# Kernel optimization log

Measured on AMD Instinct MI355X. Metric: run time of the kernel, lower is better.

## Reference

```python
import jax, jax.numpy as jnp
import numpy as np

N_NODES = 50000
N_EDGES = 800000
IN_FEATS = 512
NUM_HEADS = 4
OUT_FEATS = 64
NEG_SLOPE = 0.2


def setup_inputs() -> dict:
    key = jax.random.key(0)
    k1, k2, k3, k4, k5, k6 = jax.random.split(key, 6)
    feat = jax.random.normal(k1, (N_NODES, IN_FEATS), dtype=jnp.float32)
    W = jax.random.normal(k2, (IN_FEATS, NUM_HEADS * OUT_FEATS), dtype=jnp.float32) * (1.0 / np.sqrt(IN_FEATS))
    attn_l = jax.random.normal(k3, (NUM_HEADS, OUT_FEATS), dtype=jnp.float32) * (1.0 / np.sqrt(OUT_FEATS))
    attn_r = jax.random.normal(k4, (NUM_HEADS, OUT_FEATS), dtype=jnp.float32) * (1.0 / np.sqrt(OUT_FEATS))
    src = jax.random.randint(k5, (N_EDGES,), 0, N_NODES, dtype=jnp.int32)
    dst = jax.random.randint(k6, (N_EDGES,), 0, N_NODES, dtype=jnp.int32)
    return {"feat": feat, "W": W, "attn_l": attn_l, "attn_r": attn_r, "src": src, "dst": dst}


def reference(feat, W, attn_l, attn_r, src, dst):
    N = feat.shape[0]
    H, D = attn_l.shape
    # node-wise projection: fc(feat).view(N, H, D)
    ft = (feat @ W).reshape(N, H, D)
    # per-node attention logits
    el = jnp.einsum('nhd,hd->nh', ft, attn_l)  # [N, H]
    er = jnp.einsum('nhd,hd->nh', ft, attn_r)  # [N, H]
    # edge-wise score: leaky_relu(el[u] + er[v])
    e = jax.nn.leaky_relu(el[src] + er[dst], negative_slope=NEG_SLOPE)  # [E, H]
    # segment softmax over incoming edges of each destination node
    e_max = jax.ops.segment_max(e, dst, num_segments=N)  # [N, H]
    e_max = jnp.where(jnp.isfinite(e_max), e_max, 0.0)
    exp_e = jnp.exp(e - e_max[dst])  # [E, H]
    denom = jax.ops.segment_sum(exp_e, dst, num_segments=N)  # [N, H]
    a = exp_e / denom[dst]  # [E, H]
    # weighted message aggregation: sum_u a(u,v) * ft[u]
    msg = ft[src] * a[:, :, None]  # [E, H, D]
    out = jax.ops.segment_sum(msg, dst, num_segments=N)  # [N, H, D]
    return out.reshape(N, H * D)
```

## Files before the change

### kernel.cpp

```cpp
#include <hip/hip_runtime.h>

#define N_NODES 50000
#define N_EDGES 800000
#define IN_F    512
#define NH      4
#define DH      64
#define HD      256
#define NEG     0.2f
#define NB      ((N_NODES + 255) / 256)

typedef __attribute__((ext_vector_type(8))) short bf16x8;
typedef __attribute__((ext_vector_type(4))) float f32x4;

__device__ __forceinline__ unsigned short f2bf(float x) {
    unsigned u = __float_as_uint(x);
    unsigned r = (u + 0x7FFFu + ((u >> 16) & 1u)) >> 16;
    return (unsigned short)r;
}
__device__ __forceinline__ float bf2f(unsigned short b) {
    return __uint_as_float((unsigned)b << 16);
}

__global__ __launch_bounds__(256) void setup_kernel(const float* __restrict__ W,
                                                    unsigned short* __restrict__ WtbT,
                                                    int* __restrict__ counts) {
    int b = blockIdx.x;
    if (b < NB) {
        int i = b * 256 + threadIdx.x;
        if (i < N_NODES) counts[i] = 0;
    } else {
        int i = (b - NB) * 256 + threadIdx.x;
        if (i < IN_F * HD) {
            int k = i >> 8;
            int n = i & 255;
            int t  = k >> 6;
            int kk = k & 63;
            int g  = kk >> 3;
            int w8 = kk & 7;
            int p  = n * 8 + (g ^ (n & 7));
            WtbT[(size_t)t * 16384 + p * 8 + w8] = f2bf(W[i]);
        }
    }
}

__global__ __launch_bounds__(256) void count_kernel(const int* __restrict__ dst,
                                                    int* __restrict__ counts) {
    int e = blockIdx.x * blockDim.x + threadIdx.x;
    if (e < N_EDGES) atomicAdd(&counts[dst[e]], 1);
}

#define LDPA 72
__global__ __launch_bounds__(256) void gemm_kernel(const float* __restrict__ A,
                                                   const unsigned short* __restrict__ WtbT,
                                                   const float* __restrict__ attn_l,
                                                   const float* __restrict__ attn_r,
                                                   unsigned short* __restrict__ Cb,
                                                   float* __restrict__ el,
                                                   float* __restrict__ er) {
    __shared__ short A_s[64][LDPA];
    __shared__ short B_s[2][256 * 64];

    const int tid  = threadIdx.x;
    const int lane = tid & 63;
    const int w    = tid >> 6;
    const int lm   = lane & 15;
    const int quad = lane >> 4;
    const int row0 = blockIdx.x * 64;

    const int srow = tid >> 3;
    const int sc8  = (tid & 7) * 8;

    f32x4 acc[4][4] = {};
    float4 pa[4];

#define STAGE_B(BUF, T)                                                         \
    {                                                                           \
        const char* gsrc = (const char*)WtbT + (size_t)(T) * 32768 + tid * 16;  \
        char* ldst = (char*)&B_s[BUF][0] + tid * 16;                            \
        _Pragma("unroll")                                                       \
        for (int r = 0; r < 8; r++)                                             \
            __builtin_amdgcn_global_load_lds(                                   \
                (const __attribute__((address_space(1))) unsigned int*)(gsrc + r * 4096), \
                (__attribute__((address_space(3))) unsigned int*)(ldst + r * 4096),       \
                16, 0, 0);                                                      \
    }

#define LOAD_A(KT)                                                             \
    {                                                                          \
        int g0 = row0 + srow;                                                  \
        if (g0 < N_NODES) {                                                    \
            const float* ap = A + (size_t)g0 * IN_F + (KT) + sc8;              \
            pa[0] = *(const float4*)ap; pa[1] = *(const float4*)(ap + 4);      \
        } else { pa[0] = pa[1] = make_float4(0.f, 0.f, 0.f, 0.f); }            \
        int g1 = row0 + 32 + srow;                                             \
        if (g1 < N_NODES) {                                                    \
            const float* ap = A + (size_t)g1 * IN_F + (KT) + sc8;              \
            pa[2] = *(const float4*)ap; pa[3] = *(const float4*)(ap + 4);      \
        } else { pa[2] = pa[3] = make_float4(0.f, 0.f, 0.f, 0.f); }            \
    }

    STAGE_B(0, 0);
    LOAD_A(0);

    int buf = 0;
    for (int t = 0; t < 8; t++) {
        {
            bf16x8 s;
            s[0] = (short)f2bf(pa[0].x); s[1] = (short)f2bf(pa[0].y);
            s[2] = (short)f2bf(pa[0].z); s[3] = (short)f2bf(pa[0].w);
            s[4] = (short)f2bf(pa[1].x); s[5] = (short)f2bf(pa[1].y);
            s[6] = (short)f2bf(pa[1].z); s[7] = (short)f2bf(pa[1].w);
            *(bf16x8*)(&A_s[srow][sc8]) = s;
            s[0] = (short)f2bf(pa[2].x); s[1] = (short)f2bf(pa[2].y);
            s[2] = (short)f2bf(pa[2].z); s[3] = (short)f2bf(pa[2].w);
            s[4] = (short)f2bf(pa[3].x); s[5] = (short)f2bf(pa[3].y);
            s[6] = (short)f2bf(pa[3].z); s[7] = (short)f2bf(pa[3].w);
            *(bf16x8*)(&A_s[32 + srow][sc8]) = s;
        }
        __syncthreads();

        if (t + 1 < 8) { STAGE_B(buf ^ 1, t + 1); LOAD_A((t + 1) * 64); }

#pragma unroll
        for (int kk = 0; kk < 64; kk += 32) {
            bf16x8 af[4], bfr[4];
#pragma unroll
            for (int i = 0; i < 4; i++)
                af[i] = *(const bf16x8*)(&A_s[i * 16 + lm][kk + quad * 8]);
#pragma unroll
            for (int j = 0; j < 4; j++) {
                int n  = w * 64 + j * 16 + lm;
                int g  = (kk >> 3) + quad;
                int gs = g ^ (lm & 7);
                bfr[j] = *(const bf16x8*)(&B_s[buf][(n * 8 + gs) * 8]);
            }
#pragma unroll
            for (int i = 0; i < 4; i++)
#pragma unroll
                for (int j = 0; j < 4; j++)
                    acc[i][j] = __builtin_amdgcn_mfma_f32_16x16x32_bf16(
                        af[i], bfr[j], acc[i][j], 0, 0, 0);
        }
        if (t < 7) __syncthreads();
        buf ^= 1;
    }
#undef LOAD_A
#undef STAGE_B

#pragma unroll
    for (int i = 0; i < 4; i++) {
#pragma unroll
        for (int j = 0; j < 4; j++) {
            int gcol = w * 64 + j * 16 + lm;
#pragma unroll
            for (int r = 0; r < 4; r++) {
                int grow = row0 + i * 16 + quad * 4 + r;
                if (grow < N_NODES)
                    Cb[(size_t)grow * HD + gcol] = f2bf(acc[i][j][r]);
            }
        }
    }

    {
        float al[4], ar[4];
#pragma unroll
        for (int j = 0; j < 4; j++) {
            al[j] = attn_l[w * DH + j * 16 + lm];
            ar[j] = attn_r[w * DH + j * 16 + lm];
        }
#pragma unroll
        for (int i = 0; i < 4; i++) {
#pragma unroll
            for (int r = 0; r < 4; r++) {
                float sl = 0.f, sr = 0.f;
#pragma unroll
                for (int j = 0; j < 4; j++) {
                    sl += acc[i][j][r] * al[j];
                    sr += acc[i][j][r] * ar[j];
                }
#pragma unroll
                for (int off = 8; off > 0; off >>= 1) {
                    sl += __shfl_xor(sl, off);
                    sr += __shfl_xor(sr, off);
                }
                if (lm == 0) {
                    int grow = row0 + i * 16 + quad * 4 + r;
                    if (grow < N_NODES) {
                        el[(size_t)grow * NH + w] = sl;
                        er[(size_t)grow * NH + w] = sr;
                    }
                }
            }
        }
    }
}

__global__ __launch_bounds__(256) void partial_kernel(const int* __restrict__ counts,
                                                      int* __restrict__ bsums) {
    __shared__ int red[4];
    int i = blockIdx.x * 256 + threadIdx.x;
    int c = (i < N_NODES) ? counts[i] : 0;
#pragma unroll
    for (int off = 32; off > 0; off >>= 1) c += __shfl_down(c, off);
    if ((threadIdx.x & 63) == 0) red[threadIdx.x >> 6] = c;
    __syncthreads();
    if (threadIdx.x == 0) bsums[blockIdx.x] = red[0] + red[1] + red[2] + red[3];
}

__global__ __launch_bounds__(256) void bscan_kernel(const int* __restrict__ bsums,
                                                    int* __restrict__ boffs) {
    __shared__ int s[256];
    int tid = threadIdx.x;
    s[tid] = (tid < NB) ? bsums[tid] : 0;
    __syncthreads();
    for (int off = 1; off < 256; off <<= 1) {
        int x = s[tid];
        int a = (tid >= off) ? s[tid - off] : 0;
        __syncthreads();
        s[tid] = x + a;
        __syncthreads();
    }
    if (tid < NB) boffs[tid] = (tid > 0) ? s[tid - 1] : 0;
}

__global__ __launch_bounds__(256) void scatter_scan_kernel(const int* __restrict__ counts,
                                                           const int* __restrict__ boffs,
                                                           int* __restrict__ offsets,
                                                           int* __restrict__ cursor) {
    __shared__ int s[256];
    int tid = threadIdx.x;
    int i = blockIdx.x * 256 + tid;
    s[tid] = (i < N_NODES) ? counts[i] : 0;
    __syncthreads();
    for (int off = 1; off < 256; off <<= 1) {
        int x = s[tid];
        int a = (tid >= off) ? s[tid - off] : 0;
        __syncthreads();
        s[tid] = x + a;
        __syncthreads();
    }
    int excl = (tid > 0) ? s[tid - 1] : 0;
    int o = boffs[blockIdx.x] + excl;
    if (i < N_NODES) { offsets[i] = o; cursor[i] = o; }
    if (i == 0) offsets[N_NODES] = N_EDGES;
}

__global__ __launch_bounds__(256) void edge_place_kernel(const int* __restrict__ src,
                                                         const int* __restrict__ dst,
                                                         int* __restrict__ cursor,
                                                         int* __restrict__ srcs) {
    int e = blockIdx.x * blockDim.x + threadIdx.x;
    if (e >= N_EDGES) return;
    int u = src[e], v = dst[e];
    int pos = atomicAdd(&cursor[v], 1);
    srcs[pos] = u;
}

__device__ __forceinline__ float lrelu_exp(float x) {
    float y = fmaxf(x, NEG * x);
    return __expf(y);
}

__global__ __launch_bounds__(256) void agg_kernel(const unsigned short* __restrict__ ftb,
                                                  const float* __restrict__ el,
                                                  const float* __restrict__ er,
                                                  const int* __restrict__ srcs,
                                                  const int* __restrict__ offsets,
                                                  float* __restrict__ out) {
    int wv   = (blockIdx.x * blockDim.x + threadIdx.x) >> 6;
    int lane = threadIdx.x & 63;
    if (wv >= N_NODES) return;

    const int beg = offsets[wv];
    const int end = offsets[wv + 1];
    const int h   = lane >> 4;
    const size_t foff = (size_t)lane * 4;
    const float erv = er[(size_t)wv * NH + h];

    float4 acc = make_float4(0.f, 0.f, 0.f, 0.f);
    float dsum = 0.f;

    const int n8 = (end - beg) >> 3;
    int u0, u1, u2, u3, u4, u5, u6, u7;
    if (n8 > 0) {
        const int* sp = srcs + beg;
        u0 = sp[0]; u1 = sp[1]; u2 = sp[2]; u3 = sp[3];
        u4 = sp[4]; u5 = sp[5]; u6 = sp[6]; u7 = sp[7];
        for (int b = 0; b < n8; b++) {
            const int base = beg + b * 8;
            int v0 = 0, v1 = 0, v2 = 0, v3 = 0, v4 = 0, v5 = 0, v6 = 0, v7 = 0;
            if (b + 1 < n8) {
                const int* np = srcs + base + 8;
                v0 = np[0]; v1 = np[1]; v2 = np[2]; v3 = np[3];
                v4 = np[4]; v5 = np[5]; v6 = np[6]; v7 = np[7];
            }
            ushort4 f0 = *(const ushort4*)(ftb + (size_t)u0 * HD + foff);
            ushort4 f1 = *(const ushort4*)(ftb + (size_t)u1 * HD + foff);
            ushort4 f2 = *(const ushort4*)(ftb + (size_t)u2 * HD + foff);
            ushort4 f3 = *(const ushort4*)(ftb + (size_t)u3 * HD + foff);
            ushort4 f4 = *(const ushort4*)(ftb + (size_t)u4 * HD + foff);
            ushort4 f5 = *(const ushort4*)(ftb + (size_t)u5 * HD + foff);
            ushort4 f6 = *(const ushort4*)(ftb + (size_t)u6 * HD + foff);
            ushort4 f7 = *(const ushort4*)(ftb + (size_t)u7 * HD + foff);
            float e0 = el[(size_t)u0 * NH + h];
            float e1 = el[(size_t)u1 * NH + h];
            float e2 = el[(size_t)u2 * NH + h];
            float e3 = el[(size_t)u3 * NH + h];
            float e4 = el[(size_t)u4 * NH + h];
            float e5 = el[(size_t)u5 * NH + h];
            float e6 = el[(size_t)u6 * NH + h];
            float e7 = el[(size_t)u7 * NH + h];
            float w0 = lrelu_exp(e0 + erv), w1 = lrelu_exp(e1 + erv);
            float w2 = lrelu_exp(e2 + erv), w3 = lrelu_exp(e3 + erv);
            float w4 = lrelu_exp(e4 + erv), w5 = lrelu_exp(e5 + erv);
            float w6 = lrelu_exp(e6 + erv), w7 = lrelu_exp(e7 + erv);
            acc.x += w0 * bf2f(f0.x) + w1 * bf2f(f1.x) + w2 * bf2f(f2.x) + w3 * bf2f(f3.x)
                   + w4 * bf2f(f4.x) + w5 * bf2f(f5.x) + w6 * bf2f(f6.x) + w7 * bf2f(f7.x);
            acc.y += w0 * bf2f(f0.y) + w1 * bf2f(f1.y) + w2 * bf2f(f2.y) + w3 * bf2f(f3.y)
                   + w4 * bf2f(f4.y) + w5 * bf2f(f5.y) + w6 * bf2f(f6.y) + w7 * bf2f(f7.y);
            acc.z += w0 * bf2f(f0.z) + w1 * bf2f(f1.z) + w2 * bf2f(f2.z) + w3 * bf2f(f3.z)
                   + w4 * bf2f(f4.z) + w5 * bf2f(f5.z) + w6 * bf2f(f6.z) + w7 * bf2f(f7.z);
            acc.w += w0 * bf2f(f0.w) + w1 * bf2f(f1.w) + w2 * bf2f(f2.w) + w3 * bf2f(f3.w)
                   + w4 * bf2f(f4.w) + w5 * bf2f(f5.w) + w6 * bf2f(f6.w) + w7 * bf2f(f7.w);
            dsum += ((w0 + w1) + (w2 + w3)) + ((w4 + w5) + (w6 + w7));
            u0 = v0; u1 = v1; u2 = v2; u3 = v3;
            u4 = v4; u5 = v5; u6 = v6; u7 = v7;
        }
    }
    {
        const int p0  = beg + n8 * 8;
        const int rem = end - p0;
        if (rem > 0) {
            const int* sp = srcs + p0;
            int x0 = sp[0];
            int x1 = (1 < rem) ? sp[1] : x0;
            int x2 = (2 < rem) ? sp[2] : x0;
            int x3 = (3 < rem) ? sp[3] : x0;
            int x4 = (4 < rem) ? sp[4] : x0;
            int x5 = (5 < rem) ? sp[5] : x0;
            int x6 = (6 < rem) ? sp[6] : x0;
            ushort4 f0 = *(const ushort4*)(ftb + (size_t)x0 * HD + foff);
            ushort4 f1 = *(const ushort4*)(ftb + (size_t)x1 * HD + foff);
            ushort4 f2 = *(const ushort4*)(ftb + (size_t)x2 * HD + foff);
            ushort4 f3 = *(const ushort4*)(ftb + (size_t)x3 * HD + foff);
            ushort4 f4 = *(const ushort4*)(ftb + (size_t)x4 * HD + foff);
            ushort4 f5 = *(const ushort4*)(ftb + (size_t)x5 * HD + foff);
            ushort4 f6 = *(const ushort4*)(ftb + (size_t)x6 * HD + foff);
            float e0 = el[(size_t)x0 * NH + h];
            float e1 = el[(size_t)x1 * NH + h];
            float e2 = el[(size_t)x2 * NH + h];
            float e3 = el[(size_t)x3 * NH + h];
            float e4 = el[(size_t)x4 * NH + h];
            float e5 = el[(size_t)x5 * NH + h];
            float e6 = el[(size_t)x6 * NH + h];
            float w0 = lrelu_exp(e0 + erv);
            float w1 = (1 < rem) ? lrelu_exp(e1 + erv) : 0.f;
            float w2 = (2 < rem) ? lrelu_exp(e2 + erv) : 0.f;
            float w3 = (3 < rem) ? lrelu_exp(e3 + erv) : 0.f;
            float w4 = (4 < rem) ? lrelu_exp(e4 + erv) : 0.f;
            float w5 = (5 < rem) ? lrelu_exp(e5 + erv) : 0.f;
            float w6 = (6 < rem) ? lrelu_exp(e6 + erv) : 0.f;
            acc.x += w0 * bf2f(f0.x) + w1 * bf2f(f1.x) + w2 * bf2f(f2.x) + w3 * bf2f(f3.x)
                   + w4 * bf2f(f4.x) + w5 * bf2f(f5.x) + w6 * bf2f(f6.x);
            acc.y += w0 * bf2f(f0.y) + w1 * bf2f(f1.y) + w2 * bf2f(f2.y) + w3 * bf2f(f3.y)
                   + w4 * bf2f(f4.y) + w5 * bf2f(f5.y) + w6 * bf2f(f6.y);
            acc.z += w0 * bf2f(f0.z) + w1 * bf2f(f1.z) + w2 * bf2f(f2.z) + w3 * bf2f(f3.z)
                   + w4 * bf2f(f4.z) + w5 * bf2f(f5.z) + w6 * bf2f(f6.z);
            acc.w += w0 * bf2f(f0.w) + w1 * bf2f(f1.w) + w2 * bf2f(f2.w) + w3 * bf2f(f3.w)
                   + w4 * bf2f(f4.w) + w5 * bf2f(f5.w) + w6 * bf2f(f6.w);
            dsum += ((w0 + w1) + (w2 + w3)) + ((w4 + w5) + w6);
        }
    }

    float inv = (dsum > 0.f) ? (1.f / dsum) : 0.f;
    acc.x *= inv; acc.y *= inv; acc.z *= inv; acc.w *= inv;
    *(float4*)(out + (size_t)wv * HD + foff) = acc;
}

extern "C" void kernel_launch(void* const* d_in, const int* in_sizes, int n_in,
                              void* d_out, int out_size, void* d_ws, size_t ws_size,
                              hipStream_t stream) {
    const float* feat   = (const float*)d_in[0];
    const float* W      = (const float*)d_in[1];
    const float* attn_l = (const float*)d_in[2];
    const float* attn_r = (const float*)d_in[3];
    const int*   src    = (const int*)d_in[4];
    const int*   dst    = (const int*)d_in[5];
    float* out = (float*)d_out;

    char* p = (char*)d_ws;
    auto alloc = [&](size_t bytes) -> char* {
        char* r = p;
        p += (bytes + 255) & ~(size_t)255;
        return r;
    };
    unsigned short* ftb     = (unsigned short*)alloc((size_t)N_NODES * HD * 2);
    unsigned short* WtbT    = (unsigned short*)alloc((size_t)IN_F * HD * 2);
    float*          el      = (float*)alloc((size_t)N_NODES * NH * 4);
    float*          er      = (float*)alloc((size_t)N_NODES * NH * 4);
    int*            srcs    = (int*)alloc((size_t)N_EDGES * 4);
    int*            counts  = (int*)alloc((size_t)N_NODES * 4);
    int*            offsets = (int*)alloc((size_t)(N_NODES + 1) * 4);
    int*            cursor  = (int*)alloc((size_t)N_NODES * 4);
    int*            bsums   = (int*)alloc((size_t)NB * 4);
    int*            boffs   = (int*)alloc((size_t)NB * 4);

    setup_kernel<<<NB + (IN_F * HD + 255) / 256, 256, 0, stream>>>(W, WtbT, counts);
    count_kernel<<<(N_EDGES + 255) / 256, 256, 0, stream>>>(dst, counts);
    gemm_kernel<<<(N_NODES + 63) / 64, 256, 0, stream>>>(feat, WtbT, attn_l, attn_r,
                                                         ftb, el, er);
    partial_kernel<<<NB, 256, 0, stream>>>(counts, bsums);
    bscan_kernel<<<1, 256, 0, stream>>>(bsums, boffs);
    scatter_scan_kernel<<<NB, 256, 0, stream>>>(counts, boffs, offsets, cursor);
    edge_place_kernel<<<(N_EDGES + 255) / 256, 256, 0, stream>>>(src, dst, cursor, srcs);
    agg_kernel<<<(N_NODES + 3) / 4, 256, 0, stream>>>(ftb, el, er, srcs, offsets, out);
}
```

Baseline: 345.6 us.

## Fuse CSR build and weight prep into one cooperative kernel with grid syncs

Merges the setup, count, partial-sum, block-scan, scan-scatter and edge-placement kernels into a single cooperative kernel of 512 blocks that separates its phases with grid.sync. This removes five kernel launches and the gaps between them before the GEMM. The cost is grid-wide barriers, a fixed 512-block grid that must be co-resident, and grid-stride loops in place of full-width grids. It also drops the overlap the separate kernels might have had.

Measured after the change: 626.0 us. 1.81x slower.

```diff
diff --git a/kernel.cpp b/kernel.cpp
--- a/kernel.cpp
+++ b/kernel.cpp
@@ -1,4 +1,7 @@
 #include <hip/hip_runtime.h>
+#include <hip/hip_cooperative_groups.h>
+
+namespace cg = cooperative_groups;
 
 #define N_NODES 50000
 #define N_EDGES 800000
@@ -8,6 +11,7 @@
 #define HD      256
 #define NEG     0.2f
 #define NB      ((N_NODES + 255) / 256)
+#define BUILD_BLOCKS 512
 
 typedef __attribute__((ext_vector_type(8))) short bf16x8;
 typedef __attribute__((ext_vector_type(4))) float f32x4;
@@ -21,32 +25,86 @@
     return __uint_as_float((unsigned)b << 16);
 }
 
-__global__ __launch_bounds__(256) void setup_kernel(const float* __restrict__ W,
+__global__ __launch_bounds__(256) void build_kernel(const float* __restrict__ W,
                                                     unsigned short* __restrict__ WtbT,
-                                                    int* __restrict__ counts) {
-    int b = blockIdx.x;
-    if (b < NB) {
-        int i = b * 256 + threadIdx.x;
-        if (i < N_NODES) counts[i] = 0;
-    } else {
-        int i = (b - NB) * 256 + threadIdx.x;
-        if (i < IN_F * HD) {
-            int k = i >> 8;
-            int n = i & 255;
-            int t  = k >> 6;
-            int kk = k & 63;
-            int g  = kk >> 3;
-            int w8 = kk & 7;
-            int p  = n * 8 + (g ^ (n & 7));
-            WtbT[(size_t)t * 16384 + p * 8 + w8] = f2bf(W[i]);
-        }
-    }
-}
-
-__global__ __launch_bounds__(256) void count_kernel(const int* __restrict__ dst,
-                                                    int* __restrict__ counts) {
-    int e = blockIdx.x * blockDim.x + threadIdx.x;
-    if (e < N_EDGES) atomicAdd(&counts[dst[e]], 1);
+                                                    const int* __restrict__ src,
+                                                    const int* __restrict__ dst,
+                                                    int* __restrict__ counts,
+                                                    int* __restrict__ offsets,
+                                                    int* __restrict__ cursor,
+                                                    int* __restrict__ bsums,
+                                                    int* __restrict__ boffs,
+                                                    int* __restrict__ srcs) {
+    cg::grid_group grid = cg::this_grid();
+    __shared__ int s[256];
+    const int tid = threadIdx.x;
+    const int bid = blockIdx.x;
+    const int gthread = bid * 256 + tid;
+    const int gsz = BUILD_BLOCKS * 256;
+
+    for (int i = gthread; i < N_NODES; i += gsz) counts[i] = 0;
+    for (int i = gthread; i < IN_F * HD; i += gsz) {
+        int k = i >> 8;
+        int n = i & 255;
+        int t  = k >> 6;
+        int kk = k & 63;
+        int g  = kk >> 3;
+        int w8 = kk & 7;
+        int p  = n * 8 + (g ^ (n & 7));
+        WtbT[(size_t)t * 16384 + p * 8 + w8] = f2bf(W[i]);
+    }
+    grid.sync();
+
+    for (int e = gthread; e < N_EDGES; e += gsz) atomicAdd(&counts[dst[e]], 1);
+    grid.sync();
+
+    if (bid < NB) {
+        int i = bid * 256 + tid;
+        int c = (i < N_NODES) ? counts[i] : 0;
+        s[tid] = c;
+        __syncthreads();
+        for (int off = 1; off < 256; off <<= 1) {
+            int x = s[tid];
+            int a = (tid >= off) ? s[tid - off] : 0;
+            __syncthreads();
+            s[tid] = x + a;
+            __syncthreads();
+        }
+        if (i < N_NODES) offsets[i] = (tid > 0) ? s[tid - 1] : 0;
+        if (tid == 0) bsums[bid] = s[255];
+    }
+    grid.sync();
+
+    if (bid == 0) {
+        s[tid] = (tid < NB) ? bsums[tid] : 0;
+        __syncthreads();
+        for (int off = 1; off < 256; off <<= 1) {
+            int x = s[tid];
+            int a = (tid >= off) ? s[tid - off] : 0;
+            __syncthreads();
+            s[tid] = x + a;
+            __syncthreads();
+        }
+        if (tid < NB) boffs[tid] = (tid > 0) ? s[tid - 1] : 0;
+    }
+    grid.sync();
+
+    if (bid < NB) {
+        int i = bid * 256 + tid;
+        if (i < N_NODES) {
+            int o = offsets[i] + boffs[bid];
+            offsets[i] = o;
+            cursor[i]  = o;
+        }
+    }
+    if (gthread == 0) offsets[N_NODES] = N_EDGES;
+    grid.sync();
+
+    for (int e = gthread; e < N_EDGES; e += gsz) {
+        int u = src[e], v = dst[e];
+        int pos = atomicAdd(&cursor[v], 1);
+        srcs[pos] = u;
+    }
 }
 
 #define LDPA 72
@@ -193,67 +251,6 @@
             }
         }
     }
-}
-
-__global__ __launch_bounds__(256) void partial_kernel(const int* __restrict__ counts,
-                                                      int* __restrict__ bsums) {
-    __shared__ int red[4];
-    int i = blockIdx.x * 256 + threadIdx.x;
-    int c = (i < N_NODES) ? counts[i] : 0;
-#pragma unroll
-    for (int off = 32; off > 0; off >>= 1) c += __shfl_down(c, off);
-    if ((threadIdx.x & 63) == 0) red[threadIdx.x >> 6] = c;
-    __syncthreads();
-    if (threadIdx.x == 0) bsums[blockIdx.x] = red[0] + red[1] + red[2] + red[3];
-}
-
-__global__ __launch_bounds__(256) void bscan_kernel(const int* __restrict__ bsums,
-                                                    int* __restrict__ boffs) {
-    __shared__ int s[256];
-    int tid = threadIdx.x;
-    s[tid] = (tid < NB) ? bsums[tid] : 0;
-    __syncthreads();
-    for (int off = 1; off < 256; off <<= 1) {
-        int x = s[tid];
-        int a = (tid >= off) ? s[tid - off] : 0;
-        __syncthreads();
-        s[tid] = x + a;
-        __syncthreads();
-    }
-    if (tid < NB) boffs[tid] = (tid > 0) ? s[tid - 1] : 0;
-}
-
-__global__ __launch_bounds__(256) void scatter_scan_kernel(const int* __restrict__ counts,
-                                                           const int* __restrict__ boffs,
-                                                           int* __restrict__ offsets,
-                                                           int* __restrict__ cursor) {
-    __shared__ int s[256];
-    int tid = threadIdx.x;
-    int i = blockIdx.x * 256 + tid;
-    s[tid] = (i < N_NODES) ? counts[i] : 0;
-    __syncthreads();
-    for (int off = 1; off < 256; off <<= 1) {
-        int x = s[tid];
-        int a = (tid >= off) ? s[tid - off] : 0;
-        __syncthreads();
-        s[tid] = x + a;
-        __syncthreads();
-    }
-    int excl = (tid > 0) ? s[tid - 1] : 0;
-    int o = boffs[blockIdx.x] + excl;
-    if (i < N_NODES) { offsets[i] = o; cursor[i] = o; }
-    if (i == 0) offsets[N_NODES] = N_EDGES;
-}
-
-__global__ __launch_bounds__(256) void edge_place_kernel(const int* __restrict__ src,
-                                                         const int* __restrict__ dst,
-                                                         int* __restrict__ cursor,
-                                                         int* __restrict__ srcs) {
-    int e = blockIdx.x * blockDim.x + threadIdx.x;
-    if (e >= N_EDGES) return;
-    int u = src[e], v = dst[e];
-    int pos = atomicAdd(&cursor[v], 1);
-    srcs[pos] = u;
 }
 
 __device__ __forceinline__ float lrelu_exp(float x) {
@@ -405,13 +402,14 @@
     int*            bsums   = (int*)alloc((size_t)NB * 4);
     int*            boffs   = (int*)alloc((size_t)NB * 4);
 
-    setup_kernel<<<NB + (IN_F * HD + 255) / 256, 256, 0, stream>>>(W, WtbT, counts);
-    count_kernel<<<(N_EDGES + 255) / 256, 256, 0, stream>>>(dst, counts);
+    {
+        void* args[] = {(void*)&W, (void*)&WtbT, (void*)&src, (void*)&dst,
+                        (void*)&counts, (void*)&offsets, (void*)&cursor,
+                        (void*)&bsums, (void*)&boffs, (void*)&srcs};
+        hipLaunchCooperativeKernel((const void*)build_kernel, dim3(BUILD_BLOCKS),
+                                   dim3(256), args, 0, stream);
+    }
     gemm_kernel<<<(N_NODES + 63) / 64, 256, 0, stream>>>(feat, WtbT, attn_l, attn_r,
                                                          ftb, el, er);
-    partial_kernel<<<NB, 256, 0, stream>>>(counts, bsums);
-    bscan_kernel<<<1, 256, 0, stream>>>(bsums, boffs);
-    scatter_scan_kernel<<<NB, 256, 0, stream>>>(counts, boffs, offsets, cursor);
-    edge_place_kernel<<<(N_EDGES + 255) / 256, 256, 0, stream>>>(src, dst, cursor, srcs);
     agg_kernel<<<(N_NODES + 3) / 4, 256, 0, stream>>>(ftb, el, er, srcs, offsets, out);
 }
```
